# Kernel tuning notes

Hardware: AMD Instinct MI355X
Metric: run time of the kernel (lower is better)

## Reference

```python
import jax, jax.numpy as jnp
import numpy as np

NUM_HEADS = 12
EPS = 1e-5


def setup_inputs() -> dict:
    key = jax.random.key(0)
    k0, k1, k2 = jax.random.split(key, 3)
    B, C, D = 2, 768, 14  # batch, hidden_size, img_size//16
    x = jax.random.normal(k0, (B, C, D, D, D), dtype=jnp.float32)
    norm_w = jnp.ones((C,), dtype=jnp.float32)
    norm_b = jnp.zeros((C,), dtype=jnp.float32)
    qkv_w = jax.random.normal(k1, (3 * C, C), dtype=jnp.float32) * 0.02
    out_w = jax.random.normal(k2, (C, C), dtype=jnp.float32) * 0.02
    out_b = jnp.zeros((C,), dtype=jnp.float32)
    return {"x": x, "norm_w": norm_w, "norm_b": norm_b,
            "qkv_w": qkv_w, "out_w": out_w, "out_b": out_b}


def reference(x, norm_w, norm_b, qkv_w, out_w, out_b):
    B, C, D, H, W = x.shape
    nh = NUM_HEADS
    dh = C // nh
    scale = dh ** -0.5

    # b c d h w -> b (d h w) c
    t = jnp.transpose(x, (0, 2, 3, 4, 1)).reshape(B, D * H * W, C)
    N = t.shape[1]

    # LayerNorm over channel dim
    mu = jnp.mean(t, axis=-1, keepdims=True)
    var = jnp.mean(jnp.square(t - mu), axis=-1, keepdims=True)
    tn = (t - mu) / jnp.sqrt(var + EPS) * norm_w + norm_b

    # qkv projection (no bias), split as (3, heads, dim_head)
    qkv = tn @ qkv_w.T                       # [B, N, 3C]
    qkv = qkv.reshape(B, N, 3, nh, dh)
    qkv = jnp.transpose(qkv, (2, 0, 3, 1, 4))  # [3, B, nh, N, dh]
    q, k, v = qkv[0], qkv[1], qkv[2]

    att = jax.nn.softmax(jnp.einsum('blxn,blyn->blxy', q, k) * scale, axis=-1)
    out = jnp.einsum('blxy,blyn->blxn', att, v)  # [B, nh, N, dh]

    out = jnp.transpose(out, (0, 2, 1, 3)).reshape(B, N, C)
    out = out @ out_w.T + out_b

    out = out.reshape(B, D, H, W, C)
    out = jnp.transpose(out, (0, 4, 1, 2, 3))  # b d h w c -> b c d h w
    return out + x
```

## Files before the change

kernel.cpp:

```cpp
#include <hip/hip_runtime.h>

typedef unsigned short u16;
typedef unsigned int u32;

#define SPA 2744
#define CH  768
#define NH  12
#define DH  64
#define BB  2
#define TC  2304
#define MTOT (BB*SPA)
#define CVTB 2304

typedef __bf16 bf16x8_t __attribute__((ext_vector_type(8)));
typedef __bf16 bf16x4_t __attribute__((ext_vector_type(4)));
typedef short  s16x4    __attribute__((ext_vector_type(4)));
typedef float  f32x4_t  __attribute__((ext_vector_type(4)));

static __device__ __forceinline__ u16 f2bf(float f) {
    union { float f; u32 u; } v; v.f = f;
    u32 u = v.u;
    u += 0x7fffu + ((u >> 16) & 1u);
    return (u16)(u >> 16);
}

static __device__ __forceinline__ void gld16(const u16* g, u16* l) {
    __builtin_amdgcn_global_load_lds(
        (const __attribute__((address_space(1))) u32*)(size_t)g,
        (__attribute__((address_space(3))) u32*)(u32)(size_t)l, 16, 0, 0);
}

__global__ __launch_bounds__(256) void cvtln_kernel(const float* __restrict__ qkv_w,
                                                    u16* __restrict__ qkvw_bf, int n4a,
                                                    const float* __restrict__ out_w,
                                                    u16* __restrict__ outw_bf,
                                                    const float* __restrict__ x,
                                                    const float* __restrict__ w,
                                                    const float* __restrict__ bta,
                                                    u16* __restrict__ tn) {
    int tid = threadIdx.x;
    if (blockIdx.x < CVTB) {
        int i = blockIdx.x * 256 + tid;
        const float* src; u16* dst; int idx;
        if (i < n4a) { src = qkv_w; dst = qkvw_bf; idx = i; }
        else { src = out_w; dst = outw_bf; idx = i - n4a; }
        float4 f = ((const float4*)src)[idx];
        uint2 o;
        o.x = (u32)f2bf(f.x) | ((u32)f2bf(f.y) << 16);
        o.y = (u32)f2bf(f.z) | ((u32)f2bf(f.w) << 16);
        ((uint2*)dst)[idx] = o;
        return;
    }
    int bid = blockIdx.x - CVTB;
    __shared__ f32x4_t redS[4][16];
    __shared__ f32x4_t redQ[4][16];
    __shared__ u16 T[32][68];
    int grp = tid & 15, chl = tid >> 4;
    int wvi = tid >> 6, l16g = tid & 15;
    (void)l16g;
    int tok0 = bid * 64 + grp * 4;
    int gb = (tok0 + 3 < MTOT) ? tok0 : (MTOT - 4);
    int b = gb / SPA, n = gb - b * SPA;
    const float* base = x + (size_t)b * CH * SPA + n;

    f32x4_t s4 = {0.f, 0.f, 0.f, 0.f}, q4 = {0.f, 0.f, 0.f, 0.f};
    for (int c0 = 0; c0 < CH; c0 += 16) {
        float4 v = *(const float4*)(base + (size_t)(c0 + chl) * SPA);
        s4[0] += v.x; s4[1] += v.y; s4[2] += v.z; s4[3] += v.w;
        q4[0] += v.x * v.x; q4[1] += v.y * v.y; q4[2] += v.z * v.z; q4[3] += v.w * v.w;
    }
#pragma unroll
    for (int m = 16; m <= 32; m <<= 1)
#pragma unroll
        for (int e = 0; e < 4; e++) {
            s4[e] += __shfl_xor(s4[e], m);
            q4[e] += __shfl_xor(q4[e], m);
        }
    if ((tid & 63) < 16) { redS[wvi][grp] = s4; redQ[wvi][grp] = q4; }
    __syncthreads();
    f32x4_t st = redS[0][grp], qt = redQ[0][grp];
#pragma unroll
    for (int wv2 = 1; wv2 < 4; wv2++) {
        f32x4_t a = redS[wv2][grp], c = redQ[wv2][grp];
#pragma unroll
        for (int e = 0; e < 4; e++) { st[e] += a[e]; qt[e] += c[e]; }
    }
    f32x4_t mean4, rstd4;
#pragma unroll
    for (int e = 0; e < 4; e++) {
        mean4[e] = st[e] * (1.0f / CH);
        rstd4[e] = rsqrtf(qt[e] * (1.0f / CH) - mean4[e] * mean4[e] + 1e-5f);
    }

    int tokl = tid >> 2, qq = tid & 3;
    int g2 = bid * 64 + tokl;
    for (int c0 = 0; c0 < CH; c0 += 32) {
        __syncthreads();
#pragma unroll
        for (int h = 0; h < 2; h++) {
            int cc = c0 + h * 16 + chl;
            float4 v = *(const float4*)(base + (size_t)cc * SPA);
            float ws = w[cc], bs = bta[cc];
            union { u16 h4[4]; } pk;
            pk.h4[0] = f2bf((v.x - mean4[0]) * rstd4[0] * ws + bs);
            pk.h4[1] = f2bf((v.y - mean4[1]) * rstd4[1] * ws + bs);
            pk.h4[2] = f2bf((v.z - mean4[2]) * rstd4[2] * ws + bs);
            pk.h4[3] = f2bf((v.w - mean4[3]) * rstd4[3] * ws + bs);
            *(uint2*)(&T[h * 16 + chl][grp * 4]) = *(uint2*)pk.h4;
        }
        __syncthreads();
        if (g2 < MTOT) {
            union { u16 h[8]; int4 v4; } pk;
#pragma unroll
            for (int e = 0; e < 8; e++) pk.h[e] = T[qq * 8 + e][tokl];
            *(int4*)(tn + (size_t)g2 * CH + c0 + qq * 8) = pk.v4;
        }
    }
}

__global__ __launch_bounds__(256, 3) void gemm_qkv(const u16* __restrict__ A,
                                                   const u16* __restrict__ Bw,
                                                   u16* __restrict__ out0,
                                                   u16* __restrict__ out1,
                                                   u16* __restrict__ out2) {
    const int M = MTOT, K = CH;
    __shared__ __align__(16) u16 As[128 * 32];
    __shared__ __align__(16) u16 Bs[128 * 32];
    int tid = threadIdx.x;
    int m0 = blockIdx.y * 128;
    int n0 = blockIdx.x * 128;
    int wv = tid >> 6, lane = tid & 63;
    int wm = (wv >> 1) * 64, wn = (wv & 1) * 64;
    int quad = lane >> 4, l16 = lane & 15;

    f32x4_t zero = {0.f, 0.f, 0.f, 0.f};
    f32x4_t acc[4][4];
#pragma unroll
    for (int i = 0; i < 4; i++)
#pragma unroll
        for (int j = 0; j < 4; j++) acc[i][j] = zero;

    int rl = lane >> 2, pos = lane & 3;
    int sw = (l16 >> 1) & 3;
    for (int k0 = 0; k0 < K; k0 += 32) {
        __syncthreads();
#pragma unroll
        for (int p = 0; p < 2; p++) {
            int rbase = p * 64 + wv * 16;
            int row = rbase + rl;
            int gch = pos ^ ((row >> 1) & 3);
            int gm = m0 + row; if (gm >= M) gm = M - 1;
            gld16(A + (size_t)gm * K + k0 + gch * 8, As + rbase * 32);
            gld16(Bw + (size_t)(n0 + row) * K + k0 + gch * 8, Bs + rbase * 32);
        }
        __syncthreads();
        bf16x8_t af[4], bfr[4];
#pragma unroll
        for (int i = 0; i < 4; i++)
            af[i] = *(const bf16x8_t*)(As + (wm + i * 16 + l16) * 32 + ((quad ^ sw) * 8));
#pragma unroll
        for (int j = 0; j < 4; j++)
            bfr[j] = *(const bf16x8_t*)(Bs + (wn + j * 16 + l16) * 32 + ((quad ^ sw) * 8));
#pragma unroll
        for (int i = 0; i < 4; i++)
#pragma unroll
            for (int j = 0; j < 4; j++)
                acc[i][j] = __builtin_amdgcn_mfma_f32_16x16x32_bf16(af[i], bfr[j], acc[i][j], 0, 0, 0);
    }

    int which = n0 / CH;
    int rb = n0 - which * CH;
    u16* base = (which == 0) ? out0 : ((which == 1) ? out1 : out2);
    float qs = (which == 0) ? 0.18033688011112042f : 1.0f;
#pragma unroll
    for (int i = 0; i < 4; i++)
#pragma unroll
        for (int r = 0; r < 4; r++) {
            int gm = m0 + wm + i * 16 + quad * 4 + r;
            if (gm < M) {
                int b = gm / SPA, n = gm - b * SPA;
#pragma unroll
                for (int j = 0; j < 4; j++) {
                    int rem = rb + wn + j * 16 + l16;
                    int h = rem >> 6, d = rem & 63;
                    base[((size_t)(b * NH + h) * SPA + n) * DH + d] = f2bf(acc[i][j][r] * qs);
                }
            }
        }
}

__global__ __launch_bounds__(256, 4) void gemm_out(const u16* __restrict__ A,
                                                   const u16* __restrict__ Bw,
                                                   const float* __restrict__ xres,
                                                   const float* __restrict__ ob,
                                                   float* __restrict__ fout) {
    const int M = MTOT, K = CH;
    __shared__ __align__(16) u16 As[128 * 32];
    __shared__ __align__(16) u16 Bs[64 * 32];
    int tid = threadIdx.x;
    int m0 = blockIdx.y * 128;
    int n0 = blockIdx.x * 64;
    int wv = tid >> 6, lane = tid & 63;
    int wm = (wv >> 1) * 64, wn = (wv & 1) * 32;
    int quad = lane >> 4, l16 = lane & 15;

    f32x4_t zero = {0.f, 0.f, 0.f, 0.f};
    f32x4_t acc[4][2];
#pragma unroll
    for (int i = 0; i < 4; i++)
#pragma unroll
        for (int j = 0; j < 2; j++) acc[i][j] = zero;

    int rl = lane >> 2, pos = lane & 3;
    int sw = (l16 >> 1) & 3;
    for (int k0 = 0; k0 < K; k0 += 32) {
        __syncthreads();
#pragma unroll
        for (int p = 0; p < 2; p++) {
            int rbase = p * 64 + wv * 16;
            int row = rbase + rl;
            int gch = pos ^ ((row >> 1) & 3);
            int gm = m0 + row; if (gm >= M) gm = M - 1;
            gld16(A + (size_t)gm * K + k0 + gch * 8, As + rbase * 32);
        }
        {
            int row = wv * 16 + rl;
            int gch = pos ^ ((row >> 1) & 3);
            gld16(Bw + (size_t)(n0 + row) * K + k0 + gch * 8, Bs + (wv * 16) * 32);
        }
        __syncthreads();
        bf16x8_t af[4], bfr[2];
#pragma unroll
        for (int i = 0; i < 4; i++)
            af[i] = *(const bf16x8_t*)(As + (wm + i * 16 + l16) * 32 + ((quad ^ sw) * 8));
#pragma unroll
        for (int j = 0; j < 2; j++)
            bfr[j] = *(const bf16x8_t*)(Bs + (wn + j * 16 + l16) * 32 + ((quad ^ sw) * 8));
#pragma unroll
        for (int i = 0; i < 4; i++)
#pragma unroll
            for (int j = 0; j < 2; j++)
                acc[i][j] = __builtin_amdgcn_mfma_f32_16x16x32_bf16(af[i], bfr[j], acc[i][j], 0, 0, 0);
    }

#pragma unroll
    for (int i = 0; i < 4; i++) {
        int gm0 = m0 + wm + i * 16 + quad * 4;
        if (gm0 < M) {
            int b = gm0 / SPA;
            int n = gm0 - b * SPA;
#pragma unroll
            for (int j = 0; j < 2; j++) {
                int gn = n0 + wn + j * 16 + l16;
                size_t xo = ((size_t)(b * CH + gn)) * SPA + n;
                float4 xv = *(const float4*)(xres + xo);
                float bias = ob[gn];
                float4 rr;
                rr.x = xv.x + bias + acc[i][j][0];
                rr.y = xv.y + bias + acc[i][j][1];
                rr.z = xv.z + bias + acc[i][j][2];
                rr.w = xv.w + bias + acc[i][j][3];
                *(float4*)(fout + xo) = rr;
            }
        }
    }
}

__global__ __launch_bounds__(256) void vtrans_kernel(const u16* __restrict__ v,
                                                     u16* __restrict__ vt) {
    __shared__ __align__(16) u16 T[64 * 72];
    int bh = blockIdx.y;
    int n0 = blockIdx.x * 64;
    int tid = threadIdx.x;
#pragma unroll
    for (int h = 0; h < 2; h++) {
        int chunk = tid + h * 256;
        int r = chunk >> 3, cs = chunk & 7;
        int n = n0 + r;
        int4 val = make_int4(0, 0, 0, 0);
        if (n < SPA) val = *(const int4*)(v + ((size_t)bh * SPA + n) * DH + cs * 8);
        *(int4*)(T + r * 72 + cs * 8) = val;
    }
    __syncthreads();
#pragma unroll
    for (int h = 0; h < 2; h++) {
        int chunk = tid + h * 256;
        int d = chunk >> 3, cs = chunk & 7;
        int nb = n0 + cs * 8;
        if (nb < SPA) {
            union { u16 s[8]; int4 v4; } tmp;
#pragma unroll
            for (int e = 0; e < 8; e++) tmp.s[e] = T[(cs * 8 + e) * 72 + d];
            *(int4*)(vt + ((size_t)bh * DH + d) * SPA + nb) = tmp.v4;
        }
    }
}

__global__ __launch_bounds__(256, 3) void attn_kernel(const u16* __restrict__ q,
                                                      const u16* __restrict__ k,
                                                      const u16* __restrict__ vt,
                                                      u16* __restrict__ out) {
    __shared__ __align__(16) u16 Kbuf[2][96 * 64];
    __shared__ __align__(16) u16 Vbuf[2][64 * 108];
    int g = blockIdx.x;
    int xcd = g & 7, slot = g >> 3;
    int bh = xcd * 3 + slot % 3;
    int qg = slot / 3;
    int b = bh / NH, h = bh - b * NH;
    int tid = threadIdx.x;
    int wv = tid >> 6, lane = tid & 63;
    int quad = lane >> 4, l16 = lane & 15;
    int q0w = qg * 128 + wv * 32;

    const u16* qgp = q + (size_t)bh * SPA * DH;
    const u16* kg = k + (size_t)bh * SPA * DH;
    const u16* vg = vt + (size_t)bh * DH * SPA;

    bf16x8_t bq[2][2];
    int qglob[2];
#pragma unroll
    for (int qf = 0; qf < 2; qf++) {
        int qq = q0w + qf * 16 + l16;
        qglob[qf] = qq;
        int qld = (qq < SPA) ? qq : (SPA - 1);
#pragma unroll
        for (int ks = 0; ks < 2; ks++)
            bq[qf][ks] = *(const bf16x8_t*)(qgp + (size_t)qld * DH + ks * 32 + quad * 8);
    }

    f32x4_t zero = {0.f, 0.f, 0.f, 0.f};
    f32x4_t o[2][4];
#pragma unroll
    for (int qf = 0; qf < 2; qf++)
#pragma unroll
        for (int i = 0; i < 4; i++) o[qf][i] = zero;
    f32x4_t lacc[2];
    lacc[0] = zero; lacc[1] = zero;
    s16x4 ones;
    ones[0] = ones[1] = ones[2] = ones[3] = (short)0x3F80;

    int rl8 = lane >> 3, pos8 = lane & 7;
    int sw8 = l16 & 7;
    int vd = tid >> 2, vc = (tid & 3) * 24;

#pragma unroll
    for (int p = 0; p < 3; p++) {
        int rbase = p * 32 + wv * 8;
        int row = rbase + rl8;
        int gch = pos8 ^ (row & 7);
        gld16(kg + (size_t)row * DH + gch * 8, Kbuf[0] + rbase * 64);
    }
#pragma unroll
    for (int s2 = 0; s2 < 3; s2++)
        *(int4*)(Vbuf[0] + vd * 108 + vc + s2 * 8) =
            *(const int4*)(vg + (size_t)vd * SPA + vc + s2 * 8);

    for (int si = 0; si < 29; si++) {
        __syncthreads();
        int cur = si & 1, nxt = cur ^ 1;
        int kv0 = si * 96;
        bool hn = (si < 28);
        int4 vp0, vp1, vp2;
        if (hn) {
            int kb = kv0 + 96;
#pragma unroll
            for (int p = 0; p < 3; p++) {
                int rbase = p * 32 + wv * 8;
                int row = rbase + rl8;
                int gch = pos8 ^ (row & 7);
                int kr = kb + row; if (kr >= SPA) kr = SPA - 1;
                gld16(kg + (size_t)kr * DH + gch * 8, Kbuf[nxt] + rbase * 64);
            }
            int c0 = kb + vc;
            int a0 = c0;      if (a0 > SPA - 8) a0 = SPA - 8;
            int a1 = c0 + 8;  if (a1 > SPA - 8) a1 = SPA - 8;
            int a2 = c0 + 16; if (a2 > SPA - 8) a2 = SPA - 8;
            vp0 = *(const int4*)(vg + (size_t)vd * SPA + a0);
            vp1 = *(const int4*)(vg + (size_t)vd * SPA + a1);
            vp2 = *(const int4*)(vg + (size_t)vd * SPA + a2);
        }

        s16x4 bp[2][6];
#pragma unroll
        for (int i = 0; i < 6; i++) {
            const u16* krow = Kbuf[cur] + (i * 16 + l16) * 64;
            bf16x8_t ak0 = *(const bf16x8_t*)(krow + ((quad ^ sw8) * 8));
            bf16x8_t ak1 = *(const bf16x8_t*)(krow + (((4 + quad) ^ sw8) * 8));
            f32x4_t s0 = __builtin_amdgcn_mfma_f32_16x16x32_bf16(ak0, bq[0][0], zero, 0, 0, 0);
            s0 = __builtin_amdgcn_mfma_f32_16x16x32_bf16(ak1, bq[0][1], s0, 0, 0, 0);
            f32x4_t s1 = __builtin_amdgcn_mfma_f32_16x16x32_bf16(ak0, bq[1][0], zero, 0, 0, 0);
            s1 = __builtin_amdgcn_mfma_f32_16x16x32_bf16(ak1, bq[1][1], s1, 0, 0, 0);
            bf16x4_t p0, p1;
            if (si != 28) {
#pragma unroll
                for (int r = 0; r < 4; r++) {
                    p0[r] = (__bf16)__builtin_amdgcn_exp2f(s0[r]);
                    p1[r] = (__bf16)__builtin_amdgcn_exp2f(s1[r]);
                }
            } else {
#pragma unroll
                for (int r = 0; r < 4; r++) {
                    float e0 = __builtin_amdgcn_exp2f(s0[r]);
                    float e1 = __builtin_amdgcn_exp2f(s1[r]);
                    bool bad = (kv0 + i * 16 + quad * 4 + r) >= SPA;
                    p0[r] = (__bf16)(bad ? 0.f : e0);
                    p1[r] = (__bf16)(bad ? 0.f : e1);
                }
            }
            union { bf16x4_t b; s16x4 s; } u0, u1;
            u0.b = p0; u1.b = p1;
            bp[0][i] = u0.s; bp[1][i] = u1.s;
        }

        if (hn) {
            *(int4*)(Vbuf[nxt] + vd * 108 + vc)      = vp0;
            *(int4*)(Vbuf[nxt] + vd * 108 + vc + 8)  = vp1;
            *(int4*)(Vbuf[nxt] + vd * 108 + vc + 16) = vp2;
        }

#pragma unroll
        for (int c = 0; c < 6; c++) {
            lacc[0] = __builtin_amdgcn_mfma_f32_16x16x16bf16_1k(ones, bp[0][c], lacc[0], 0, 0, 0);
            lacc[1] = __builtin_amdgcn_mfma_f32_16x16x16bf16_1k(ones, bp[1][c], lacc[1], 0, 0, 0);
#pragma unroll
            for (int i = 0; i < 4; i++) {
                s16x4 av = *(const s16x4*)(Vbuf[cur] + (i * 16 + l16) * 108 + c * 16 + quad * 4);
                o[0][i] = __builtin_amdgcn_mfma_f32_16x16x16bf16_1k(av, bp[0][c], o[0][i], 0, 0, 0);
                o[1][i] = __builtin_amdgcn_mfma_f32_16x16x16bf16_1k(av, bp[1][c], o[1][i], 0, 0, 0);
            }
        }
    }

#pragma unroll
    for (int qf = 0; qf < 2; qf++) {
        int qq = qglob[qf];
        if (qq < SPA) {
            float inv = 1.0f / lacc[qf][0];
            u16* op = out + ((size_t)(b * SPA + qq)) * CH + h * DH;
#pragma unroll
            for (int i = 0; i < 4; i++) {
                bf16x4_t ov;
#pragma unroll
                for (int r = 0; r < 4; r++) ov[r] = (__bf16)(o[qf][i][r] * inv);
                *(bf16x4_t*)(op + i * 16 + quad * 4) = ov;
            }
        }
    }
}

extern "C" void kernel_launch(void* const* d_in, const int* in_sizes, int n_in,
                              void* d_out, int out_size, void* d_ws, size_t ws_size,
                              hipStream_t stream) {
    const float* x      = (const float*)d_in[0];
    const float* norm_w = (const float*)d_in[1];
    const float* norm_b = (const float*)d_in[2];
    const float* qkv_w  = (const float*)d_in[3];
    const float* out_w  = (const float*)d_in[4];
    const float* out_b  = (const float*)d_in[5];
    float* out = (float*)d_out;

    char* ws = (char*)d_ws;
    size_t off = 0;
    auto alloc = [&](size_t bytes) -> void* {
        void* p = ws + off;
        off += (bytes + 255) & ~(size_t)255;
        return p;
    };
    u16* tn      = (u16*)alloc((size_t)MTOT * CH * 2);
    u16* qkvw_bf = (u16*)alloc((size_t)TC * CH * 2);
    u16* outw_bf = (u16*)alloc((size_t)CH * CH * 2);
    u16* qb      = (u16*)alloc((size_t)BB * NH * SPA * DH * 2);
    u16* kb      = (u16*)alloc((size_t)BB * NH * SPA * DH * 2);
    u16* vb      = (u16*)alloc((size_t)BB * NH * SPA * DH * 2);
    u16* vtb     = (u16*)alloc((size_t)BB * NH * SPA * DH * 2);
    u16* ao      = (u16*)alloc((size_t)MTOT * CH * 2);

    int n4a = TC * CH / 4;
    cvtln_kernel<<<CVTB + (MTOT + 63) / 64, 256, 0, stream>>>(
        qkv_w, qkvw_bf, n4a, out_w, outw_bf, x, norm_w, norm_b, tn);
    gemm_qkv<<<dim3(TC / 128, (MTOT + 127) / 128), 256, 0, stream>>>(
        tn, qkvw_bf, qb, kb, vb);
    vtrans_kernel<<<dim3((SPA + 63) / 64, BB * NH), 256, 0, stream>>>(vb, vtb);
    attn_kernel<<<528, 256, 0, stream>>>(qb, kb, vtb, ao);
    gemm_out<<<dim3(CH / 64, (MTOT + 127) / 128), 256, 0, stream>>>(
        ao, outw_bf, x, out_b, out);
}
```

Baseline: 248.8 us.

## Split attention KV tiles across wave pairs and reduce partials in shared memory

Each block now handles 64 queries instead of 128. The four waves form two query halves times two KV halves: each wave processes 48 of the 96 keys per tile. The partial O accumulators and row sums are combined through LDS at the end. The grid roughly doubles (528 to 1032 blocks), raising parallelism and balancing work across CUs. In exchange, each K/V tile is reused by half as many queries, so global K/V traffic doubles, and a shared-memory reduction plus extra barriers are added.

```diff
diff --git a/kernel.cpp b/kernel.cpp
--- a/kernel.cpp
+++ b/kernel.cpp
@@ -310,7 +310,9 @@
     int tid = threadIdx.x;
     int wv = tid >> 6, lane = tid & 63;
     int quad = lane >> 4, l16 = lane & 15;
-    int q0w = qg * 128 + wv * 32;
+    int qhalf = wv & 1, khalf = wv >> 1;
+    int koff = khalf * 48;
+    int q0w = qg * 64 + qhalf * 32;
 
     const u16* qgp = q + (size_t)bh * SPA * DH;
     const u16* kg = k + (size_t)bh * SPA * DH;
@@ -380,10 +382,10 @@
             vp2 = *(const int4*)(vg + (size_t)vd * SPA + a2);
         }
 
-        s16x4 bp[2][6];
-#pragma unroll
-        for (int i = 0; i < 6; i++) {
-            const u16* krow = Kbuf[cur] + (i * 16 + l16) * 64;
+        s16x4 bp[2][3];
+#pragma unroll
+        for (int i = 0; i < 3; i++) {
+            const u16* krow = Kbuf[cur] + (koff + i * 16 + l16) * 64;
             bf16x8_t ak0 = *(const bf16x8_t*)(krow + ((quad ^ sw8) * 8));
             bf16x8_t ak1 = *(const bf16x8_t*)(krow + (((4 + quad) ^ sw8) * 8));
             f32x4_t s0 = __builtin_amdgcn_mfma_f32_16x16x32_bf16(ak0, bq[0][0], zero, 0, 0, 0);
@@ -402,7 +404,7 @@
                 for (int r = 0; r < 4; r++) {
                     float e0 = __builtin_amdgcn_exp2f(s0[r]);
                     float e1 = __builtin_amdgcn_exp2f(s1[r]);
-                    bool bad = (kv0 + i * 16 + quad * 4 + r) >= SPA;
+                    bool bad = (kv0 + koff + i * 16 + quad * 4 + r) >= SPA;
                     p0[r] = (__bf16)(bad ? 0.f : e0);
                     p1[r] = (__bf16)(bad ? 0.f : e1);
                 }
@@ -419,30 +421,57 @@
         }
 
 #pragma unroll
-        for (int c = 0; c < 6; c++) {
+        for (int c = 0; c < 3; c++) {
             lacc[0] = __builtin_amdgcn_mfma_f32_16x16x16bf16_1k(ones, bp[0][c], lacc[0], 0, 0, 0);
             lacc[1] = __builtin_amdgcn_mfma_f32_16x16x16bf16_1k(ones, bp[1][c], lacc[1], 0, 0, 0);
 #pragma unroll
             for (int i = 0; i < 4; i++) {
-                s16x4 av = *(const s16x4*)(Vbuf[cur] + (i * 16 + l16) * 108 + c * 16 + quad * 4);
+                s16x4 av = *(const s16x4*)(Vbuf[cur] + (i * 16 + l16) * 108 + koff + c * 16 + quad * 4);
                 o[0][i] = __builtin_amdgcn_mfma_f32_16x16x16bf16_1k(av, bp[0][c], o[0][i], 0, 0, 0);
                 o[1][i] = __builtin_amdgcn_mfma_f32_16x16x16bf16_1k(av, bp[1][c], o[1][i], 0, 0, 0);
             }
         }
     }
 
-#pragma unroll
-    for (int qf = 0; qf < 2; qf++) {
-        int qq = qglob[qf];
-        if (qq < SPA) {
-            float inv = 1.0f / lacc[qf][0];
-            u16* op = out + ((size_t)(b * SPA + qq)) * CH + h * DH;
+    __syncthreads();
+    float* lsh = (float*)Kbuf;
+    if (wv >= 2) {
+        int base = ((wv - 2) * 64 + lane) * 36;
+#pragma unroll
+        for (int qf = 0; qf < 2; qf++)
+#pragma unroll
+            for (int i = 0; i < 4; i++)
+                *(f32x4_t*)(lsh + base + qf * 16 + i * 4) = o[qf][i];
+        lsh[base + 32] = lacc[0][0];
+        lsh[base + 33] = lacc[1][0];
+    }
+    __syncthreads();
+    if (wv < 2) {
+        int base = (wv * 64 + lane) * 36;
+#pragma unroll
+        for (int qf = 0; qf < 2; qf++)
 #pragma unroll
             for (int i = 0; i < 4; i++) {
-                bf16x4_t ov;
-#pragma unroll
-                for (int r = 0; r < 4; r++) ov[r] = (__bf16)(o[qf][i][r] * inv);
-                *(bf16x4_t*)(op + i * 16 + quad * 4) = ov;
+                f32x4_t t = *(const f32x4_t*)(lsh + base + qf * 16 + i * 4);
+#pragma unroll
+                for (int r = 0; r < 4; r++) o[qf][i][r] += t[r];
+            }
+        float lsum[2];
+        lsum[0] = lacc[0][0] + lsh[base + 32];
+        lsum[1] = lacc[1][0] + lsh[base + 33];
+#pragma unroll
+        for (int qf = 0; qf < 2; qf++) {
+            int qq = qglob[qf];
+            if (qq < SPA) {
+                float inv = 1.0f / lsum[qf];
+                u16* op = out + ((size_t)(b * SPA + qq)) * CH + h * DH;
+#pragma unroll
+                for (int i = 0; i < 4; i++) {
+                    bf16x4_t ov;
+#pragma unroll
+                    for (int r = 0; r < 4; r++) ov[r] = (__bf16)(o[qf][i][r] * inv);
+                    *(bf16x4_t*)(op + i * 16 + quad * 4) = ov;
+                }
             }
         }
     }
@@ -481,7 +510,7 @@
     gemm_qkv<<<dim3(TC / 128, (MTOT + 127) / 128), 256, 0, stream>>>(
         tn, qkvw_bf, qb, kb, vb);
     vtrans_kernel<<<dim3((SPA + 63) / 64, BB * NH), 256, 0, stream>>>(vb, vtb);
-    attn_kernel<<<528, 256, 0, stream>>>(qb, kb, vtb, ao);
+    attn_kernel<<<1032, 256, 0, stream>>>(qb, kb, vtb, ao);
     gemm_out<<<dim3(CH / 64, (MTOT + 127) / 128), 256, 0, stream>>>(
         ao, outw_bf, x, out_b, out);
 }
```

Result: no change. 247.5 us (-0.5%).
